# Kernel tuning notes

Measured on AMD Instinct MI355X. Metric: run time of the kernel, lower is better.

## Reference

```python
import jax, jax.numpy as jnp
import numpy as np

B, S, I, H = 1024, 512, 1, 50  # batch, seq_len, input_size, hidden_size


def setup_inputs() -> dict:
    key = jax.random.key(0)
    ks = jax.random.split(key, 7)
    s_ih = 1.0 / np.sqrt(H)
    return {
        "x": jax.random.normal(ks[0], (B, S, I), dtype=jnp.float32),
        "h0": jnp.zeros((1, B, H), dtype=jnp.float32),
        "c0": jnp.zeros((1, B, H), dtype=jnp.float32),
        # PyTorch nn.LSTM params, gate order [i, f, g, o]
        "W_ih": jax.random.uniform(ks[1], (4 * H, I), jnp.float32, -s_ih, s_ih),
        "W_hh": jax.random.uniform(ks[2], (4 * H, H), jnp.float32, -s_ih, s_ih),
        "b_ih": jax.random.uniform(ks[3], (4 * H,), jnp.float32, -s_ih, s_ih),
        "b_hh": jax.random.uniform(ks[4], (4 * H,), jnp.float32, -s_ih, s_ih),
        "fc_w": jax.random.uniform(ks[5], (1, H), jnp.float32, -s_ih, s_ih),
        "fc_b": jax.random.uniform(ks[6], (1,), jnp.float32, -s_ih, s_ih),
    }


def reference(x, h0, c0, W_ih, W_hh, b_ih, b_hh, fc_w, fc_b):
    # Precompute the input projection for all timesteps: [B, S, 4H] -> scan over S
    x_proj = jnp.einsum("bsi,gi->bsg", x, W_ih) + (b_ih + b_hh)
    x_proj = jnp.transpose(x_proj, (1, 0, 2))  # [S, B, 4H]

    def step(carry, xp_t):
        h, c = carry  # each [B, H]
        gates = xp_t + h @ W_hh.T  # [B, 4H]
        i_g, f_g, g_g, o_g = jnp.split(gates, 4, axis=-1)
        c_new = jax.nn.sigmoid(f_g) * c + jax.nn.sigmoid(i_g) * jnp.tanh(g_g)
        h_new = jax.nn.sigmoid(o_g) * jnp.tanh(c_new)
        return (h_new, c_new), None

    (h_n, c_n), _ = jax.lax.scan(step, (h0[0], c0[0]), x_proj)
    # out[:, -1, :] is the final hidden state; fc head: [B, H] -> [B, 1]
    out = h_n @ fc_w.T + fc_b
    return out, h_n[None], c_n[None]
```

## Files before the change

kernel.cpp:

```cpp
#include <hip/hip_runtime.h>


typedef _Float16 half2v __attribute__((ext_vector_type(2)));

#define LOG2E 1.44269504088896340736f
#define B_ 1024
#define S_ 512
#define H_ 50

__device__ __forceinline__ float rcp_(float x) { return __builtin_amdgcn_rcpf(x); }
__device__ __forceinline__ float ex2_(float x) { return __builtin_amdgcn_exp2f(x); }

__global__ void lstm_pack(const float* __restrict__ W_ih, const float* __restrict__ W_hh,
                          const float* __restrict__ b_ih, const float* __restrict__ b_hh,
                          unsigned* __restrict__ wpk, float* __restrict__ wih_pk,
                          float* __restrict__ bias_pk)
{
    int tid = blockIdx.x * blockDim.x + threadIdx.x;
    int stride = blockDim.x * gridDim.x;
    for (int p = tid; p < 4 * 25 * 64; p += stride) {
        int j = p & 63;
        int m = (p >> 6) % 25;
        int g = p / (25 * 64);
        float s = (g == 2) ? (2.0f * LOG2E) : (-LOG2E);
        float a = 0.0f, bb = 0.0f;
        if (j < H_) {
            int row = g * H_ + j;
            a  = s * W_hh[row * H_ + 2 * m];
            bb = s * W_hh[row * H_ + 2 * m + 1];
        }
        half2v hv;
        hv.x = (_Float16)a;
        hv.y = (_Float16)bb;
        wpk[p] = __builtin_bit_cast(unsigned, hv);
    }
    for (int p = tid; p < 4 * 64; p += stride) {
        int j = p & 63;
        int g = p >> 6;
        float s = (g == 2) ? (2.0f * LOG2E) : (-LOG2E);
        float wi = 0.0f, bb = 0.0f;
        if (j < H_) {
            int row = g * H_ + j;
            wi = s * W_ih[row];
            bb = s * (b_ih[row] + b_hh[row]);
        }
        wih_pk[p] = wi;
        bias_pk[p] = bb;
    }
}

__global__
__attribute__((amdgpu_flat_work_group_size(64, 64)))
__attribute__((amdgpu_waves_per_eu(1, 1)))
void lstm_main(const float* __restrict__ x, const float* __restrict__ h0,
               const float* __restrict__ c0, const float* __restrict__ fc_w,
               const float* __restrict__ fc_b, const unsigned* __restrict__ wpk,
               const float* __restrict__ wih_pk, const float* __restrict__ bias_pk,
               float* __restrict__ out)
{
    const int b = blockIdx.x;
    const int j = threadIdx.x;

    __shared__ unsigned hs16[32];

    half2v w0[25], w1[25], w2[25], w3[25];
    #pragma unroll
    for (int m = 0; m < 25; ++m) {
        w0[m] = __builtin_bit_cast(half2v, wpk[(0 * 25 + m) * 64 + j]);
        w1[m] = __builtin_bit_cast(half2v, wpk[(1 * 25 + m) * 64 + j]);
        w2[m] = __builtin_bit_cast(half2v, wpk[(2 * 25 + m) * 64 + j]);
        w3[m] = __builtin_bit_cast(half2v, wpk[(3 * 25 + m) * 64 + j]);
    }

    float wih0 = wih_pk[0 * 64 + j], wih1 = wih_pk[1 * 64 + j];
    float wih2 = wih_pk[2 * 64 + j], wih3 = wih_pk[3 * 64 + j];
    float bs0 = bias_pk[0 * 64 + j], bs1 = bias_pk[1 * 64 + j];
    float bs2 = bias_pk[2 * 64 + j], bs3 = bias_pk[3 * 64 + j];

    float h = (j < H_) ? h0[b * H_ + j] : 0.0f;
    float c = (j < H_) ? c0[b * H_ + j] : 0.0f;

    {
        int hn_ = __builtin_amdgcn_update_dpp(0, __builtin_bit_cast(int, h),
                                              0xB1, 0xF, 0xF, true);
        unsigned hpk = __builtin_bit_cast(unsigned,
            __builtin_amdgcn_cvt_pkrtz(h, __builtin_bit_cast(float, hn_)));
        if ((j & 1) == 0 && j < H_ + 1) hs16[j >> 1] = hpk;
    }
    unsigned hp[25];
    #pragma unroll
    for (int m = 0; m < 25; ++m) hp[m] = hs16[m];

    const float* __restrict__ xrow = x + b * S_;
    float xt = xrow[0];

    for (int s = 0; s < S_; ++s) {
        int sn = s + 1 < S_ ? s + 1 : S_ - 1;
        float xt_n = xrow[sn];

        float a0 = __builtin_fmaf(xt, wih0, bs0);
        float a1 = __builtin_fmaf(xt, wih1, bs1);
        float a2 = __builtin_fmaf(xt, wih2, bs2);
        float a3 = __builtin_fmaf(xt, wih3, bs3);

        #pragma unroll
        for (int m = 0; m < 25; ++m) {
            half2v hm = __builtin_bit_cast(half2v, hp[m]);
            a0 = __builtin_amdgcn_fdot2(hm, w0[m], a0, false);
            a1 = __builtin_amdgcn_fdot2(hm, w1[m], a1, false);
            a2 = __builtin_amdgcn_fdot2(hm, w2[m], a2, false);
            a3 = __builtin_amdgcn_fdot2(hm, w3[m], a3, false);
        }
        float ei = ex2_(a0); float si = rcp_(1.0f + ei);
        float ef = ex2_(a1); float sf = rcp_(1.0f + ef);
        float eg = ex2_(a2);
        float tg = __builtin_fmaf(-2.0f, rcp_(1.0f + eg), 1.0f);
        float eo = ex2_(a3); float so = rcp_(1.0f + eo);

        c = __builtin_fmaf(sf, c, si * tg);
        float ec = ex2_((2.0f * LOG2E) * c);
        float tc = __builtin_fmaf(-2.0f, rcp_(1.0f + ec), 1.0f);
        h = so * tc;

        int hn_ = __builtin_amdgcn_update_dpp(0, __builtin_bit_cast(int, h),
                                              0xB1, 0xF, 0xF, true);
        unsigned hpk = __builtin_bit_cast(unsigned,
            __builtin_amdgcn_cvt_pkrtz(h, __builtin_bit_cast(float, hn_)));
        if ((j & 1) == 0 && j < H_ + 1) hs16[j >> 1] = hpk;
        #pragma unroll
        for (int m = 0; m < 25; ++m) hp[m] = hs16[m];

        xt = xt_n;
    }

    if (j < H_) {
        out[B_ + b * H_ + j]            = h;
        out[B_ + B_ * H_ + b * H_ + j]  = c;
    }
    float p = (j < H_) ? h * fc_w[j] : 0.0f;
    #pragma unroll
    for (int off = 32; off > 0; off >>= 1) p += __shfl_xor(p, off);
    if (j == 0) out[b] = p + fc_b[0];
}

extern "C" void kernel_launch(void* const* d_in, const int* in_sizes, int n_in,
                              void* d_out, int out_size, void* d_ws, size_t ws_size,
                              hipStream_t stream)
{
    const float* x    = (const float*)d_in[0];
    const float* h0   = (const float*)d_in[1];
    const float* c0   = (const float*)d_in[2];
    const float* W_ih = (const float*)d_in[3];
    const float* W_hh = (const float*)d_in[4];
    const float* b_ih = (const float*)d_in[5];
    const float* b_hh = (const float*)d_in[6];
    const float* fc_w = (const float*)d_in[7];
    const float* fc_b = (const float*)d_in[8];
    float* out = (float*)d_out;

    unsigned* wpk  = (unsigned*)d_ws;
    float* wih_pk  = (float*)((char*)d_ws + 6400 * 4);
    float* bias_pk = (float*)((char*)d_ws + 6400 * 4 + 256 * 4);

    lstm_pack<<<16, 256, 0, stream>>>(W_ih, W_hh, b_ih, b_hh, wpk, wih_pk, bias_pk);
    lstm_main<<<B_, 64, 0, stream>>>(x, h0, c0, fc_w, fc_b, wpk, wih_pk, bias_pk, out);
}
```

Measured before the change: 198.3 us.

## Split LSTM gates across two waves per sequence with LDS exchange

```diff
diff --git a/kernel.cpp b/kernel.cpp
--- a/kernel.cpp
+++ b/kernel.cpp
@@ -10,6 +10,9 @@
 
 __device__ __forceinline__ float rcp_(float x) { return __builtin_amdgcn_rcpf(x); }
 __device__ __forceinline__ float ex2_(float x) { return __builtin_amdgcn_exp2f(x); }
+__device__ __forceinline__ float fdot2_(unsigned hp, half2v w, float acc) {
+    return __builtin_amdgcn_fdot2(__builtin_bit_cast(half2v, hp), w, acc, false);
+}
 
 __global__ void lstm_pack(const float* __restrict__ W_ih, const float* __restrict__ W_hh,
                           const float* __restrict__ b_ih, const float* __restrict__ b_hh,
@@ -50,43 +53,45 @@
 }
 
 __global__
-__attribute__((amdgpu_flat_work_group_size(64, 64)))
-__attribute__((amdgpu_waves_per_eu(1, 1)))
+__attribute__((amdgpu_flat_work_group_size(128, 128)))
+__attribute__((amdgpu_waves_per_eu(2)))
 void lstm_main(const float* __restrict__ x, const float* __restrict__ h0,
                const float* __restrict__ c0, const float* __restrict__ fc_w,
                const float* __restrict__ fc_b, const unsigned* __restrict__ wpk,
                const float* __restrict__ wih_pk, const float* __restrict__ bias_pk,
                float* __restrict__ out)
 {
-    const int b = blockIdx.x;
-    const int j = threadIdx.x;
+    const int b   = blockIdx.x;
+    const int tid = threadIdx.x;
+    const int j   = tid & 63;
+    const int wid = tid >> 6;
 
     __shared__ unsigned hs16[32];
+    __shared__ float2   sfso[64];
 
-    half2v w0[25], w1[25], w2[25], w3[25];
+    const int gA = wid;
+    const int gB = wid + 2;
+
+    half2v wA[25], wB[25];
     #pragma unroll
     for (int m = 0; m < 25; ++m) {
-        w0[m] = __builtin_bit_cast(half2v, wpk[(0 * 25 + m) * 64 + j]);
-        w1[m] = __builtin_bit_cast(half2v, wpk[(1 * 25 + m) * 64 + j]);
-        w2[m] = __builtin_bit_cast(half2v, wpk[(2 * 25 + m) * 64 + j]);
-        w3[m] = __builtin_bit_cast(half2v, wpk[(3 * 25 + m) * 64 + j]);
+        wA[m] = __builtin_bit_cast(half2v, wpk[(gA * 25 + m) * 64 + j]);
+        wB[m] = __builtin_bit_cast(half2v, wpk[(gB * 25 + m) * 64 + j]);
     }
-
-    float wih0 = wih_pk[0 * 64 + j], wih1 = wih_pk[1 * 64 + j];
-    float wih2 = wih_pk[2 * 64 + j], wih3 = wih_pk[3 * 64 + j];
-    float bs0 = bias_pk[0 * 64 + j], bs1 = bias_pk[1 * 64 + j];
-    float bs2 = bias_pk[2 * 64 + j], bs3 = bias_pk[3 * 64 + j];
+    float wihA = wih_pk[gA * 64 + j], wihB = wih_pk[gB * 64 + j];
+    float bsA  = bias_pk[gA * 64 + j], bsB = bias_pk[gB * 64 + j];
 
     float h = (j < H_) ? h0[b * H_ + j] : 0.0f;
     float c = (j < H_) ? c0[b * H_ + j] : 0.0f;
 
-    {
+    if (wid == 0) {
         int hn_ = __builtin_amdgcn_update_dpp(0, __builtin_bit_cast(int, h),
                                               0xB1, 0xF, 0xF, true);
         unsigned hpk = __builtin_bit_cast(unsigned,
             __builtin_amdgcn_cvt_pkrtz(h, __builtin_bit_cast(float, hn_)));
-        if ((j & 1) == 0 && j < H_ + 1) hs16[j >> 1] = hpk;
+        if ((j & 1) == 0 && j < H_) hs16[j >> 1] = hpk;
     }
+    __syncthreads();
     unsigned hp[25];
     #pragma unroll
     for (int m = 0; m < 25; ++m) hp[m] = hs16[m];
@@ -95,52 +100,59 @@
     float xt = xrow[0];
 
     for (int s = 0; s < S_; ++s) {
-        int sn = s + 1 < S_ ? s + 1 : S_ - 1;
-        float xt_n = xrow[sn];
+        float xt_n = xrow[s + 1 < S_ ? s + 1 : S_ - 1];
 
-        float a0 = __builtin_fmaf(xt, wih0, bs0);
-        float a1 = __builtin_fmaf(xt, wih1, bs1);
-        float a2 = __builtin_fmaf(xt, wih2, bs2);
-        float a3 = __builtin_fmaf(xt, wih3, bs3);
+        float aA1 = __builtin_fmaf(xt, wihA, bsA), aA2 = 0.0f;
+        float aB1 = __builtin_fmaf(xt, wihB, bsB), aB2 = 0.0f;
+        #pragma unroll
+        for (int m = 0; m < 13; ++m) {
+            aA1 = fdot2_(hp[m], wA[m], aA1);
+            aB1 = fdot2_(hp[m], wB[m], aB1);
+        }
+        #pragma unroll
+        for (int m = 13; m < 25; ++m) {
+            aA2 = fdot2_(hp[m], wA[m], aA2);
+            aB2 = fdot2_(hp[m], wB[m], aB2);
+        }
+        float aA = aA1 + aA2;
+        float aB = aB1 + aB2;
+
+        float eA = ex2_(aA); float sA = rcp_(1.0f + eA);
+        float eB = ex2_(aB); float rB = rcp_(1.0f + eB);
+
+        if (wid == 1 && j < H_) sfso[j] = make_float2(sA, rB);
+        __syncthreads();
+
+        if (wid == 0) {
+            float tg = __builtin_fmaf(-2.0f, rB, 1.0f);
+            float2 t = sfso[j < H_ ? j : 0];
+            c = __builtin_fmaf(t.x, c, sA * tg);
+            float ec = ex2_((2.0f * LOG2E) * c);
+            float tc = __builtin_fmaf(-2.0f, rcp_(1.0f + ec), 1.0f);
+            h = t.y * tc;
+            int hn_ = __builtin_amdgcn_update_dpp(0, __builtin_bit_cast(int, h),
+                                                  0xB1, 0xF, 0xF, true);
+            unsigned hpk = __builtin_bit_cast(unsigned,
+                __builtin_amdgcn_cvt_pkrtz(h, __builtin_bit_cast(float, hn_)));
+            if ((j & 1) == 0 && j < H_) hs16[j >> 1] = hpk;
+        }
+        __syncthreads();
 
         #pragma unroll
-        for (int m = 0; m < 25; ++m) {
-            half2v hm = __builtin_bit_cast(half2v, hp[m]);
-            a0 = __builtin_amdgcn_fdot2(hm, w0[m], a0, false);
-            a1 = __builtin_amdgcn_fdot2(hm, w1[m], a1, false);
-            a2 = __builtin_amdgcn_fdot2(hm, w2[m], a2, false);
-            a3 = __builtin_amdgcn_fdot2(hm, w3[m], a3, false);
-        }
-        float ei = ex2_(a0); float si = rcp_(1.0f + ei);
-        float ef = ex2_(a1); float sf = rcp_(1.0f + ef);
-        float eg = ex2_(a2);
-        float tg = __builtin_fmaf(-2.0f, rcp_(1.0f + eg), 1.0f);
-        float eo = ex2_(a3); float so = rcp_(1.0f + eo);
-
-        c = __builtin_fmaf(sf, c, si * tg);
-        float ec = ex2_((2.0f * LOG2E) * c);
-        float tc = __builtin_fmaf(-2.0f, rcp_(1.0f + ec), 1.0f);
-        h = so * tc;
-
-        int hn_ = __builtin_amdgcn_update_dpp(0, __builtin_bit_cast(int, h),
-                                              0xB1, 0xF, 0xF, true);
-        unsigned hpk = __builtin_bit_cast(unsigned,
-            __builtin_amdgcn_cvt_pkrtz(h, __builtin_bit_cast(float, hn_)));
-        if ((j & 1) == 0 && j < H_ + 1) hs16[j >> 1] = hpk;
-        #pragma unroll
         for (int m = 0; m < 25; ++m) hp[m] = hs16[m];
-
         xt = xt_n;
     }
 
-    if (j < H_) {
-        out[B_ + b * H_ + j]            = h;
-        out[B_ + B_ * H_ + b * H_ + j]  = c;
+    if (wid == 0) {
+        if (j < H_) {
+            out[B_ + b * H_ + j]           = h;
+            out[B_ + B_ * H_ + b * H_ + j] = c;
+        }
+        float p = (j < H_) ? h * fc_w[j] : 0.0f;
+        #pragma unroll
+        for (int off = 32; off > 0; off >>= 1) p += __shfl_xor(p, off);
+        if (j == 0) out[b] = p + fc_b[0];
     }
-    float p = (j < H_) ? h * fc_w[j] : 0.0f;
-    #pragma unroll
-    for (int off = 32; off > 0; off >>= 1) p += __shfl_xor(p, off);
-    if (j == 0) out[b] = p + fc_b[0];
 }
 
 extern "C" void kernel_launch(void* const* d_in, const int* in_sizes, int n_in,
@@ -163,5 +175,5 @@
     float* bias_pk = (float*)((char*)d_ws + 6400 * 4 + 256 * 4);
 
     lstm_pack<<<16, 256, 0, stream>>>(W_ih, W_hh, b_ih, b_hh, wpk, wih_pk, bias_pk);
-    lstm_main<<<B_, 64, 0, stream>>>(x, h0, c0, fc_w, fc_b, wpk, wih_pk, bias_pk, out);
+    lstm_main<<<B_, 128, 0, stream>>>(x, h0, c0, fc_w, fc_b, wpk, wih_pk, bias_pk, out);
 }
```

Measured after the change: 221.8 us. 1.12x slower.

## Hand-write LSTM step loop in inline asm with readlane broadcast of h

Applied to the files above, without the earlier changes.

```diff
diff --git a/kernel.cpp b/kernel.cpp
--- a/kernel.cpp
+++ b/kernel.cpp
@@ -8,20 +8,18 @@
 #define S_ 512
 #define H_ 50
 
-__device__ __forceinline__ float rcp_(float x) { return __builtin_amdgcn_rcpf(x); }
-__device__ __forceinline__ float ex2_(float x) { return __builtin_amdgcn_exp2f(x); }
-
 __global__ void lstm_pack(const float* __restrict__ W_ih, const float* __restrict__ W_hh,
                           const float* __restrict__ b_ih, const float* __restrict__ b_hh,
-                          unsigned* __restrict__ wpk, float* __restrict__ wih_pk,
+                          unsigned* __restrict__ wpk2, float* __restrict__ wih_pk,
                           float* __restrict__ bias_pk)
 {
     int tid = blockIdx.x * blockDim.x + threadIdx.x;
     int stride = blockDim.x * gridDim.x;
-    for (int p = tid; p < 4 * 25 * 64; p += stride) {
-        int j = p & 63;
-        int m = (p >> 6) % 25;
-        int g = p / (25 * 64);
+    for (int p = tid; p < 64 * 100; p += stride) {
+        int j = p / 100;
+        int r = p - j * 100;
+        int g = r / 25;
+        int m = r - g * 25;
         float s = (g == 2) ? (2.0f * LOG2E) : (-LOG2E);
         float a = 0.0f, bb = 0.0f;
         if (j < H_) {
@@ -32,7 +30,7 @@
         half2v hv;
         hv.x = (_Float16)a;
         hv.y = (_Float16)bb;
-        wpk[p] = __builtin_bit_cast(unsigned, hv);
+        wpk2[p] = __builtin_bit_cast(unsigned, hv);
     }
     for (int p = tid; p < 4 * 64; p += stride) {
         int j = p & 63;
@@ -54,24 +52,13 @@
 __attribute__((amdgpu_waves_per_eu(1, 1)))
 void lstm_main(const float* __restrict__ x, const float* __restrict__ h0,
                const float* __restrict__ c0, const float* __restrict__ fc_w,
-               const float* __restrict__ fc_b, const unsigned* __restrict__ wpk,
+               const float* __restrict__ fc_b, const unsigned* __restrict__ wpk2,
                const float* __restrict__ wih_pk, const float* __restrict__ bias_pk,
                float* __restrict__ out)
 {
     const int b = blockIdx.x;
     const int j = threadIdx.x;
 
-    __shared__ unsigned hs16[32];
-
-    half2v w0[25], w1[25], w2[25], w3[25];
-    #pragma unroll
-    for (int m = 0; m < 25; ++m) {
-        w0[m] = __builtin_bit_cast(half2v, wpk[(0 * 25 + m) * 64 + j]);
-        w1[m] = __builtin_bit_cast(half2v, wpk[(1 * 25 + m) * 64 + j]);
-        w2[m] = __builtin_bit_cast(half2v, wpk[(2 * 25 + m) * 64 + j]);
-        w3[m] = __builtin_bit_cast(half2v, wpk[(3 * 25 + m) * 64 + j]);
-    }
-
     float wih0 = wih_pk[0 * 64 + j], wih1 = wih_pk[1 * 64 + j];
     float wih2 = wih_pk[2 * 64 + j], wih3 = wih_pk[3 * 64 + j];
     float bs0 = bias_pk[0 * 64 + j], bs1 = bias_pk[1 * 64 + j];
@@ -80,64 +67,275 @@
     float h = (j < H_) ? h0[b * H_ + j] : 0.0f;
     float c = (j < H_) ? c0[b * H_ + j] : 0.0f;
 
-    {
-        int hn_ = __builtin_amdgcn_update_dpp(0, __builtin_bit_cast(int, h),
-                                              0xB1, 0xF, 0xF, true);
-        unsigned hpk = __builtin_bit_cast(unsigned,
-            __builtin_amdgcn_cvt_pkrtz(h, __builtin_bit_cast(float, hn_)));
-        if ((j & 1) == 0 && j < H_ + 1) hs16[j >> 1] = hpk;
+    int hn_ = __builtin_amdgcn_update_dpp(0, __builtin_bit_cast(int, h),
+                                          0xB1, 0xF, 0xF, true);
+    unsigned hpk0 = __builtin_bit_cast(unsigned,
+        __builtin_amdgcn_cvt_pkrtz(h, __builtin_bit_cast(float, hn_)));
+
+    unsigned long long wa = (unsigned long long)(wpk2 + (size_t)j * 100);
+    const float* xrow = x + (size_t)b * S_;
+
+    float hf, cf;
+    asm volatile(
+        "v_mov_b32 v60, %[hpk]\n\t"
+        "v_mov_b32 v61, %[h]\n\t"
+        "v_mov_b32 v62, %[c]\n\t"
+        "global_load_dwordx4 v[80:83], %[wa], off\n\t"
+        "global_load_dwordx4 v[84:87], %[wa], off offset:16\n\t"
+        "global_load_dwordx4 v[88:91], %[wa], off offset:32\n\t"
+        "global_load_dwordx4 v[92:95], %[wa], off offset:48\n\t"
+        "global_load_dwordx4 v[96:99], %[wa], off offset:64\n\t"
+        "global_load_dwordx4 v[100:103], %[wa], off offset:80\n\t"
+        "global_load_dwordx4 v[104:107], %[wa], off offset:96\n\t"
+        "global_load_dwordx4 v[108:111], %[wa], off offset:112\n\t"
+        "global_load_dwordx4 v[112:115], %[wa], off offset:128\n\t"
+        "global_load_dwordx4 v[116:119], %[wa], off offset:144\n\t"
+        "global_load_dwordx4 v[120:123], %[wa], off offset:160\n\t"
+        "global_load_dwordx4 v[124:127], %[wa], off offset:176\n\t"
+        "global_load_dwordx4 v[128:131], %[wa], off offset:192\n\t"
+        "global_load_dwordx4 v[132:135], %[wa], off offset:208\n\t"
+        "global_load_dwordx4 v[136:139], %[wa], off offset:224\n\t"
+        "global_load_dwordx4 v[140:143], %[wa], off offset:240\n\t"
+        "global_load_dwordx4 v[144:147], %[wa], off offset:256\n\t"
+        "global_load_dwordx4 v[148:151], %[wa], off offset:272\n\t"
+        "global_load_dwordx4 v[152:155], %[wa], off offset:288\n\t"
+        "global_load_dwordx4 v[156:159], %[wa], off offset:304\n\t"
+        "global_load_dwordx4 v[160:163], %[wa], off offset:320\n\t"
+        "global_load_dwordx4 v[164:167], %[wa], off offset:336\n\t"
+        "global_load_dwordx4 v[168:171], %[wa], off offset:352\n\t"
+        "global_load_dwordx4 v[172:175], %[wa], off offset:368\n\t"
+        "global_load_dwordx4 v[176:179], %[wa], off offset:384\n\t"
+        "s_mov_b32 s18, 0\n\t"
+        "s_load_dword s17, %[xp], s18\n\t"
+        "s_movk_i32 s16, 0x200\n\t"
+        "s_waitcnt vmcnt(0) lgkmcnt(0)\n\t"
+        "s_mov_b32 s21, s17\n\t"
+        "v_readlane_b32 s24, v60, 0\n\t"
+        "v_readlane_b32 s25, v60, 2\n\t"
+        "v_readlane_b32 s26, v60, 4\n\t"
+        "v_readlane_b32 s27, v60, 6\n\t"
+        "v_readlane_b32 s28, v60, 8\n\t"
+        "v_readlane_b32 s29, v60, 10\n\t"
+        "Lstep_%=:\n\t"
+        "s_add_u32 s18, s18, 4\n\t"
+        "s_min_u32 s19, s18, 0x7FC\n\t"
+        "s_load_dword s17, %[xp], s19\n\t"
+        "v_fma_f32 v64, s21, %[wih0], %[bs0]\n\t"
+        "v_fma_f32 v65, s21, %[wih1], %[bs1]\n\t"
+        "v_fma_f32 v66, s21, %[wih2], %[bs2]\n\t"
+        "v_fma_f32 v67, s21, %[wih3], %[bs3]\n\t"
+        "v_mov_b32 v40, s24\n\t"
+        "v_mov_b32 v41, s25\n\t"
+        "v_mov_b32 v42, s26\n\t"
+        "v_readlane_b32 s30, v60, 12\n\t"
+        "v_mov_b32 v43, s27\n\t"
+        "v_dot2_f32_f16 v64, v40, v80, v64\n\t"
+        "v_dot2_f32_f16 v65, v40, v105, v65\n\t"
+        "v_dot2_f32_f16 v66, v40, v130, v66\n\t"
+        "v_dot2_f32_f16 v67, v40, v155, v67\n\t"
+        "v_readlane_b32 s31, v60, 14\n\t"
+        "v_mov_b32 v44, s28\n\t"
+        "v_dot2_f32_f16 v64, v41, v81, v64\n\t"
+        "v_dot2_f32_f16 v65, v41, v106, v65\n\t"
+        "v_dot2_f32_f16 v66, v41, v131, v66\n\t"
+        "v_dot2_f32_f16 v67, v41, v156, v67\n\t"
+        "v_readlane_b32 s24, v60, 16\n\t"
+        "v_mov_b32 v45, s29\n\t"
+        "v_dot2_f32_f16 v64, v42, v82, v64\n\t"
+        "v_dot2_f32_f16 v65, v42, v107, v65\n\t"
+        "v_dot2_f32_f16 v66, v42, v132, v66\n\t"
+        "v_dot2_f32_f16 v67, v42, v157, v67\n\t"
+        "v_readlane_b32 s25, v60, 18\n\t"
+        "v_mov_b32 v46, s30\n\t"
+        "v_dot2_f32_f16 v64, v43, v83, v64\n\t"
+        "v_dot2_f32_f16 v65, v43, v108, v65\n\t"
+        "v_dot2_f32_f16 v66, v43, v133, v66\n\t"
+        "v_dot2_f32_f16 v67, v43, v158, v67\n\t"
+        "v_readlane_b32 s26, v60, 20\n\t"
+        "v_mov_b32 v47, s31\n\t"
+        "v_dot2_f32_f16 v64, v44, v84, v64\n\t"
+        "v_dot2_f32_f16 v65, v44, v109, v65\n\t"
+        "v_dot2_f32_f16 v66, v44, v134, v66\n\t"
+        "v_dot2_f32_f16 v67, v44, v159, v67\n\t"
+        "v_readlane_b32 s27, v60, 22\n\t"
+        "v_mov_b32 v40, s24\n\t"
+        "v_dot2_f32_f16 v64, v45, v85, v64\n\t"
+        "v_dot2_f32_f16 v65, v45, v110, v65\n\t"
+        "v_dot2_f32_f16 v66, v45, v135, v66\n\t"
+        "v_dot2_f32_f16 v67, v45, v160, v67\n\t"
+        "v_readlane_b32 s28, v60, 24\n\t"
+        "v_mov_b32 v41, s25\n\t"
+        "v_dot2_f32_f16 v64, v46, v86, v64\n\t"
+        "v_dot2_f32_f16 v65, v46, v111, v65\n\t"
+        "v_dot2_f32_f16 v66, v46, v136, v66\n\t"
+        "v_dot2_f32_f16 v67, v46, v161, v67\n\t"
+        "v_readlane_b32 s29, v60, 26\n\t"
+        "v_mov_b32 v42, s26\n\t"
+        "v_dot2_f32_f16 v64, v47, v87, v64\n\t"
+        "v_dot2_f32_f16 v65, v47, v112, v65\n\t"
+        "v_dot2_f32_f16 v66, v47, v137, v66\n\t"
+        "v_dot2_f32_f16 v67, v47, v162, v67\n\t"
+        "v_readlane_b32 s30, v60, 28\n\t"
+        "v_mov_b32 v43, s27\n\t"
+        "v_dot2_f32_f16 v64, v40, v88, v64\n\t"
+        "v_dot2_f32_f16 v65, v40, v113, v65\n\t"
+        "v_dot2_f32_f16 v66, v40, v138, v66\n\t"
+        "v_dot2_f32_f16 v67, v40, v163, v67\n\t"
+        "v_readlane_b32 s31, v60, 30\n\t"
+        "v_mov_b32 v44, s28\n\t"
+        "v_dot2_f32_f16 v64, v41, v89, v64\n\t"
+        "v_dot2_f32_f16 v65, v41, v114, v65\n\t"
+        "v_dot2_f32_f16 v66, v41, v139, v66\n\t"
+        "v_dot2_f32_f16 v67, v41, v164, v67\n\t"
+        "v_readlane_b32 s24, v60, 32\n\t"
+        "v_mov_b32 v45, s29\n\t"
+        "v_dot2_f32_f16 v64, v42, v90, v64\n\t"
+        "v_dot2_f32_f16 v65, v42, v115, v65\n\t"
+        "v_dot2_f32_f16 v66, v42, v140, v66\n\t"
+        "v_dot2_f32_f16 v67, v42, v165, v67\n\t"
+        "v_readlane_b32 s25, v60, 34\n\t"
+        "v_mov_b32 v46, s30\n\t"
+        "v_dot2_f32_f16 v64, v43, v91, v64\n\t"
+        "v_dot2_f32_f16 v65, v43, v116, v65\n\t"
+        "v_dot2_f32_f16 v66, v43, v141, v66\n\t"
+        "v_dot2_f32_f16 v67, v43, v166, v67\n\t"
+        "v_readlane_b32 s26, v60, 36\n\t"
+        "v_mov_b32 v47, s31\n\t"
+        "v_dot2_f32_f16 v64, v44, v92, v64\n\t"
+        "v_dot2_f32_f16 v65, v44, v117, v65\n\t"
+        "v_dot2_f32_f16 v66, v44, v142, v66\n\t"
+        "v_dot2_f32_f16 v67, v44, v167, v67\n\t"
+        "v_readlane_b32 s27, v60, 38\n\t"
+        "v_mov_b32 v40, s24\n\t"
+        "v_dot2_f32_f16 v64, v45, v93, v64\n\t"
+        "v_dot2_f32_f16 v65, v45, v118, v65\n\t"
+        "v_dot2_f32_f16 v66, v45, v143, v66\n\t"
+        "v_dot2_f32_f16 v67, v45, v168, v67\n\t"
+        "v_readlane_b32 s28, v60, 40\n\t"
+        "v_mov_b32 v41, s25\n\t"
+        "v_dot2_f32_f16 v64, v46, v94, v64\n\t"
+        "v_dot2_f32_f16 v65, v46, v119, v65\n\t"
+        "v_dot2_f32_f16 v66, v46, v144, v66\n\t"
+        "v_dot2_f32_f16 v67, v46, v169, v67\n\t"
+        "v_readlane_b32 s29, v60, 42\n\t"
+        "v_mov_b32 v42, s26\n\t"
+        "v_dot2_f32_f16 v64, v47, v95, v64\n\t"
+        "v_dot2_f32_f16 v65, v47, v120, v65\n\t"
+        "v_dot2_f32_f16 v66, v47, v145, v66\n\t"
+        "v_dot2_f32_f16 v67, v47, v170, v67\n\t"
+        "v_readlane_b32 s30, v60, 44\n\t"
+        "v_mov_b32 v43, s27\n\t"
+        "v_dot2_f32_f16 v64, v40, v96, v64\n\t"
+        "v_dot2_f32_f16 v65, v40, v121, v65\n\t"
+        "v_dot2_f32_f16 v66, v40, v146, v66\n\t"
+        "v_dot2_f32_f16 v67, v40, v171, v67\n\t"
+        "v_readlane_b32 s31, v60, 46\n\t"
+        "v_mov_b32 v44, s28\n\t"
+        "v_dot2_f32_f16 v64, v41, v97, v64\n\t"
+        "v_dot2_f32_f16 v65, v41, v122, v65\n\t"
+        "v_dot2_f32_f16 v66, v41, v147, v66\n\t"
+        "v_dot2_f32_f16 v67, v41, v172, v67\n\t"
+        "v_readlane_b32 s24, v60, 48\n\t"
+        "v_mov_b32 v45, s29\n\t"
+        "v_dot2_f32_f16 v64, v42, v98, v64\n\t"
+        "v_dot2_f32_f16 v65, v42, v123, v65\n\t"
+        "v_dot2_f32_f16 v66, v42, v148, v66\n\t"
+        "v_dot2_f32_f16 v67, v42, v173, v67\n\t"
+        "v_mov_b32 v46, s30\n\t"
+        "v_dot2_f32_f16 v64, v43, v99, v64\n\t"
+        "v_dot2_f32_f16 v65, v43, v124, v65\n\t"
+        "v_dot2_f32_f16 v66, v43, v149, v66\n\t"
+        "v_dot2_f32_f16 v67, v43, v174, v67\n\t"
+        "v_mov_b32 v47, s31\n\t"
+        "v_dot2_f32_f16 v64, v44, v100, v64\n\t"
+        "v_dot2_f32_f16 v65, v44, v125, v65\n\t"
+        "v_dot2_f32_f16 v66, v44, v150, v66\n\t"
+        "v_dot2_f32_f16 v67, v44, v175, v67\n\t"
+        "v_mov_b32 v40, s24\n\t"
+        "v_dot2_f32_f16 v64, v45, v101, v64\n\t"
+        "v_dot2_f32_f16 v65, v45, v126, v65\n\t"
+        "v_dot2_f32_f16 v66, v45, v151, v66\n\t"
+        "v_dot2_f32_f16 v67, v45, v176, v67\n\t"
+        "v_dot2_f32_f16 v64, v46, v102, v64\n\t"
+        "v_dot2_f32_f16 v65, v46, v127, v65\n\t"
+        "v_dot2_f32_f16 v66, v46, v152, v66\n\t"
+        "v_dot2_f32_f16 v67, v46, v177, v67\n\t"
+        "v_dot2_f32_f16 v64, v47, v103, v64\n\t"
+        "v_dot2_f32_f16 v65, v47, v128, v65\n\t"
+        "v_dot2_f32_f16 v66, v47, v153, v66\n\t"
+        "v_dot2_f32_f16 v67, v47, v178, v67\n\t"
+        "v_dot2_f32_f16 v64, v40, v104, v64\n\t"
+        "v_dot2_f32_f16 v65, v40, v129, v65\n\t"
+        "v_dot2_f32_f16 v66, v40, v154, v66\n\t"
+        "v_dot2_f32_f16 v67, v40, v179, v67\n\t"
+        "v_exp_f32 v68, v64\n\t"
+        "v_exp_f32 v69, v65\n\t"
+        "v_exp_f32 v70, v66\n\t"
+        "v_exp_f32 v71, v67\n\t"
+        "v_add_f32 v68, 1.0, v68\n\t"
+        "v_add_f32 v69, 1.0, v69\n\t"
+        "v_add_f32 v70, 1.0, v70\n\t"
+        "v_add_f32 v71, 1.0, v71\n\t"
+        "v_rcp_f32 v70, v70\n\t"
+        "v_rcp_f32 v68, v68\n\t"
+        "v_rcp_f32 v69, v69\n\t"
+        "v_rcp_f32 v71, v71\n\t"
+        "v_fma_f32 v72, -2.0, v70, 1.0\n\t"
+        "v_mul_f32 v72, v68, v72\n\t"
+        "v_fma_f32 v62, v69, v62, v72\n\t"
+        "v_mul_f32 v73, 0x4038aa3b, v62\n\t"
+        "v_exp_f32 v73, v73\n\t"
+        "s_nop 0\n\t"
+        "v_add_f32 v73, 1.0, v73\n\t"
+        "v_rcp_f32 v73, v73\n\t"
+        "s_nop 0\n\t"
+        "v_fma_f32 v73, -2.0, v73, 1.0\n\t"
+        "v_mul_f32 v61, v71, v73\n\t"
+        "s_waitcnt lgkmcnt(0)\n\t"
+        "s_mov_b32 s21, s17\n\t"
+        "v_mov_b32_dpp v63, v61 quad_perm:[1,0,3,2] row_mask:0xf bank_mask:0xf\n\t"
+        "v_cvt_pkrtz_f16_f32 v60, v61, v63\n\t"
+        "s_sub_u32 s16, s16, 1\n\t"
+        "v_readlane_b32 s24, v60, 0\n\t"
+        "v_readlane_b32 s25, v60, 2\n\t"
+        "v_readlane_b32 s26, v60, 4\n\t"
+        "v_readlane_b32 s27, v60, 6\n\t"
+        "v_readlane_b32 s28, v60, 8\n\t"
+        "v_readlane_b32 s29, v60, 10\n\t"
+        "s_cmp_lg_u32 s16, 0\n\t"
+        "s_cbranch_scc1 Lstep_%=\n\t"
+        "v_mov_b32 %[hf], v61\n\t"
+        "v_mov_b32 %[cf], v62\n\t"
+        : [hf] "=&v"(hf), [cf] "=&v"(cf)
+        : [h] "v"(h), [c] "v"(c), [hpk] "v"(hpk0), [wa] "v"(wa),
+          [xp] "s"(xrow),
+          [wih0] "v"(wih0), [wih1] "v"(wih1), [wih2] "v"(wih2), [wih3] "v"(wih3),
+          [bs0] "v"(bs0), [bs1] "v"(bs1), [bs2] "v"(bs2), [bs3] "v"(bs3)
+        : "memory", "scc", "vcc",
+          "s16", "s17", "s18", "s19", "s21",
+          "s24", "s25", "s26", "s27", "s28", "s29", "s30", "s31",
+          "v40", "v41", "v42", "v43", "v44", "v45", "v46", "v47",
+          "v60", "v61", "v62", "v63", "v64", "v65", "v66", "v67",
+          "v68", "v69", "v70", "v71", "v72", "v73",
+          "v80", "v81", "v82", "v83", "v84", "v85", "v86", "v87",
+          "v88", "v89", "v90", "v91", "v92", "v93", "v94", "v95",
+          "v96", "v97", "v98", "v99", "v100", "v101", "v102", "v103",
+          "v104", "v105", "v106", "v107", "v108", "v109", "v110", "v111",
+          "v112", "v113", "v114", "v115", "v116", "v117", "v118", "v119",
+          "v120", "v121", "v122", "v123", "v124", "v125", "v126", "v127",
+          "v128", "v129", "v130", "v131", "v132", "v133", "v134", "v135",
+          "v136", "v137", "v138", "v139", "v140", "v141", "v142", "v143",
+          "v144", "v145", "v146", "v147", "v148", "v149", "v150", "v151",
+          "v152", "v153", "v154", "v155", "v156", "v157", "v158", "v159",
+          "v160", "v161", "v162", "v163", "v164", "v165", "v166", "v167",
+          "v168", "v169", "v170", "v171", "v172", "v173", "v174", "v175",
+          "v176", "v177", "v178", "v179");
+
+    if (j < H_) {
+        out[B_ + b * H_ + j]           = hf;
+        out[B_ + B_ * H_ + b * H_ + j] = cf;
     }
-    unsigned hp[25];
-    #pragma unroll
-    for (int m = 0; m < 25; ++m) hp[m] = hs16[m];
-
-    const float* __restrict__ xrow = x + b * S_;
-    float xt = xrow[0];
-
-    for (int s = 0; s < S_; ++s) {
-        int sn = s + 1 < S_ ? s + 1 : S_ - 1;
-        float xt_n = xrow[sn];
-
-        float a0 = __builtin_fmaf(xt, wih0, bs0);
-        float a1 = __builtin_fmaf(xt, wih1, bs1);
-        float a2 = __builtin_fmaf(xt, wih2, bs2);
-        float a3 = __builtin_fmaf(xt, wih3, bs3);
-
-        #pragma unroll
-        for (int m = 0; m < 25; ++m) {
-            half2v hm = __builtin_bit_cast(half2v, hp[m]);
-            a0 = __builtin_amdgcn_fdot2(hm, w0[m], a0, false);
-            a1 = __builtin_amdgcn_fdot2(hm, w1[m], a1, false);
-            a2 = __builtin_amdgcn_fdot2(hm, w2[m], a2, false);
-            a3 = __builtin_amdgcn_fdot2(hm, w3[m], a3, false);
-        }
-        float ei = ex2_(a0); float si = rcp_(1.0f + ei);
-        float ef = ex2_(a1); float sf = rcp_(1.0f + ef);
-        float eg = ex2_(a2);
-        float tg = __builtin_fmaf(-2.0f, rcp_(1.0f + eg), 1.0f);
-        float eo = ex2_(a3); float so = rcp_(1.0f + eo);
-
-        c = __builtin_fmaf(sf, c, si * tg);
-        float ec = ex2_((2.0f * LOG2E) * c);
-        float tc = __builtin_fmaf(-2.0f, rcp_(1.0f + ec), 1.0f);
-        h = so * tc;
-
-        int hn_ = __builtin_amdgcn_update_dpp(0, __builtin_bit_cast(int, h),
-                                              0xB1, 0xF, 0xF, true);
-        unsigned hpk = __builtin_bit_cast(unsigned,
-            __builtin_amdgcn_cvt_pkrtz(h, __builtin_bit_cast(float, hn_)));
-        if ((j & 1) == 0 && j < H_ + 1) hs16[j >> 1] = hpk;
-        #pragma unroll
-        for (int m = 0; m < 25; ++m) hp[m] = hs16[m];
-
-        xt = xt_n;
-    }
-
-    if (j < H_) {
-        out[B_ + b * H_ + j]            = h;
-        out[B_ + B_ * H_ + b * H_ + j]  = c;
-    }
-    float p = (j < H_) ? h * fc_w[j] : 0.0f;
+    float p = (j < H_) ? hf * fc_w[j] : 0.0f;
     #pragma unroll
     for (int off = 32; off > 0; off >>= 1) p += __shfl_xor(p, off);
     if (j == 0) out[b] = p + fc_b[0];
@@ -158,10 +356,10 @@
     const float* fc_b = (const float*)d_in[8];
     float* out = (float*)d_out;
 
-    unsigned* wpk  = (unsigned*)d_ws;
+    unsigned* wpk2 = (unsigned*)d_ws;
     float* wih_pk  = (float*)((char*)d_ws + 6400 * 4);
     float* bias_pk = (float*)((char*)d_ws + 6400 * 4 + 256 * 4);
 
-    lstm_pack<<<16, 256, 0, stream>>>(W_ih, W_hh, b_ih, b_hh, wpk, wih_pk, bias_pk);
-    lstm_main<<<B_, 64, 0, stream>>>(x, h0, c0, fc_w, fc_b, wpk, wih_pk, bias_pk, out);
+    lstm_pack<<<16, 256, 0, stream>>>(W_ih, W_hh, b_ih, b_hh, wpk2, wih_pk, bias_pk);
+    lstm_main<<<B_, 64, 0, stream>>>(x, h0, c0, fc_w, fc_b, wpk2, wih_pk, bias_pk, out);
 }
```

Measured after the change: 198.8 us. About the same (+0.3%).
